# Performance work log

Measured on AMD Instinct MI355X. Metric: run time of the kernel, lower is better.

## Reference

```python
import jax, jax.numpy as jnp
import numpy as np

U, L, B = 512, 512, 256  # units, num_layers (rectangular mesh: L == U), batch
PI = float(np.pi)


def cc_mul(a, b):
    # complex multiply of stacked (real, imag) tensors
    return jnp.stack((a[0] * b[0] - a[1] * b[1], a[0] * b[1] + a[1] * b[0]))


def i_mul(c):
    # s_mul(1j, c): multiply stacked complex by 1j -> (-im, re)
    return jnp.stack((-c[1], c[0]))


def setup_inputs() -> dict:
    key = jax.random.key(0)
    ks = jax.random.split(key, 8)
    x = jax.random.normal(ks[0], (2, B, U), jnp.float32)
    two_pi = 2.0 * PI
    theta = jax.random.uniform(ks[1], (L, U // 2), jnp.float32) * two_pi
    phi = jax.random.uniform(ks[2], (L, U // 2), jnp.float32) * two_pi
    gamma = jax.random.uniform(ks[3], (U,), jnp.float32) * two_pi
    mask = jnp.ones((L, U // 2), jnp.float32)
    enn = jax.random.uniform(ks[4], (U, L), jnp.float32)
    enp = jax.random.uniform(ks[5], (U, L), jnp.float32)
    epn = jax.random.uniform(ks[6], (U, L), jnp.float32)
    epp = jax.random.uniform(ks[7], (U, L), jnp.float32)
    # rectangular-mesh permutations: identity at input/output, interior layers
    # alternate circular shifts so MZIs couple (0,1),(2,3),... then (1,2),(3,4),...
    perms = np.tile(np.arange(U, dtype=np.int32), (L + 1, 1))
    for l in range(1, L):
        perms[l] = np.roll(perms[l], 1 if l % 2 else -1)
    perms = jnp.asarray(perms)
    # pairwise off-diagonal permutation: swap adjacent pairs [1,0,3,2,...]
    pairwise_perm = jnp.asarray(
        np.arange(U, dtype=np.int32).reshape(-1, 2)[:, ::-1].ravel())
    return dict(x=x, theta=theta, phi=phi, gamma=gamma, mask=mask,
                enn=enn, enp=enp, epn=epn, epp=epp,
                perms=perms, pairwise_perm=pairwise_perm)


def reference(x, theta, phi, gamma, mask, enn, enp, epn, epp, perms, pairwise_perm):
    # --- MeshPhasesTorch (basis='sm', hadamard=False) ---
    inv = 1.0 - mask
    th = theta * mask + inv * PI  # (1 - hadamard) * pi
    ph = phi * mask + inv * PI

    def stripe(p):  # single_mode_arrangement: [L, U//2] -> [U, L]
        return jnp.zeros((U, L), p.dtype).at[::2].set(p.T)

    internal = stripe(th)
    external = stripe(ph)
    ipsl = jnp.stack((jnp.cos(internal), jnp.sin(internal)))  # [2, U, L]
    epsl = jnp.stack((jnp.cos(external), jnp.sin(external)))  # [2, U, L]

    roll_m1 = lambda t: jnp.roll(t, -1, axis=1)  # along units axis
    roll_p1 = lambda t: jnp.roll(t, 1, axis=1)

    # --- MeshTorch.mesh_layers (hadamard=False branch) ---
    s11 = epp * ipsl - enn * roll_m1(ipsl)
    s22 = roll_p1(-enn * ipsl + epp * roll_m1(ipsl))
    s12 = i_mul(roll_p1(enp * ipsl + epn * roll_m1(ipsl)))
    s21 = i_mul(epn * ipsl + enp * roll_m1(ipsl))

    diag = cc_mul(epsl, s11 + s22) * 0.5              # [2, U, L]
    off = cc_mul(roll_p1(epsl), s21 + s12) * 0.5      # [2, U, L]
    diag = jnp.transpose(diag, (0, 2, 1))             # [2, L, U]
    off = jnp.transpose(off, (0, 2, 1))

    # --- forward: input phase shift, then sequential vertical layers ---
    in_ps = jnp.stack((jnp.cos(gamma), jnp.sin(gamma)))  # [2, U]
    out = cc_mul(x, in_ps[:, None, :])                   # [2, B, U]
    out = out[..., perms[0]]                             # left perm of layer 0

    def step(carry, inp):
        d, o, rp = inp  # [2, U], [2, U], [U]
        y = cc_mul(carry, d[:, None, :]) \
            + cc_mul(carry, o[:, None, :])[..., pairwise_perm]
        return y[..., rp], None

    xs = (jnp.moveaxis(diag, 1, 0), jnp.moveaxis(off, 1, 0), perms[1:])
    out, _ = jax.lax.scan(step, out, xs)
    return out
```

## Files before the change

kernel.cpp:

```cpp
#include <hip/hip_runtime.h>
#include <hip/hip_fp16.h>


#define UU 512
#define LL 512
#define BB 256
#define KK 256
#define KF 4
#define N9 128
#define W9 9
#define N17 64
#define W17 17
#define N33 32
#define W33 33
#define GQSTRIDE 67584
#define GBLK     8192
#define GTAIL    65536


__global__ __launch_bounds__(512, 2) void mesh_build4(
    const float* __restrict__ theta, const float* __restrict__ phi,
    const float* __restrict__ enn,   const float* __restrict__ enp,
    const float* __restrict__ epn,   const float* __restrict__ epp,
    float2* __restrict__ g9)
{
    __shared__ float2 gwj[7 * UU];
    __shared__ float2 xbuf[2][UU];
    const int u  = threadIdx.x;
    const int j  = ((blockIdx.x & 7) << 4) | (blockIdx.x >> 3);
    const int um = (u + UU - 1) & (UU - 1);
    const int l0 = j * KF;

    const float4 epp_u4 = *(const float4*)(epp + u * LL + l0);
    const float4 epp_m4 = *(const float4*)(epp + um * LL + l0);
    const float4 enn_u4 = *(const float4*)(enn + u * LL + l0);
    const float4 enn_m4 = *(const float4*)(enn + um * LL + l0);
    const float4 enp_u4 = *(const float4*)(enp + u * LL + l0);
    const float4 enp_m4 = *(const float4*)(enp + um * LL + l0);
    const float4 epn_u4 = *(const float4*)(epn + u * LL + l0);
    const float4 epn_m4 = *(const float4*)(epn + um * LL + l0);
    const float epp_u8[4] = {epp_u4.x, epp_u4.y, epp_u4.z, epp_u4.w};
    const float epp_m8[4] = {epp_m4.x, epp_m4.y, epp_m4.z, epp_m4.w};
    const float enn_u8[4] = {enn_u4.x, enn_u4.y, enn_u4.z, enn_u4.w};
    const float enn_m8[4] = {enn_m4.x, enn_m4.y, enn_m4.z, enn_m4.w};
    const float enp_u8[4] = {enp_u4.x, enp_u4.y, enp_u4.z, enp_u4.w};
    const float enp_m8[4] = {enp_m4.x, enp_m4.y, enp_m4.z, enp_m4.w};
    const float epn_u8[4] = {epn_u4.x, epn_u4.y, epn_u4.z, epn_u4.w};
    const float epn_m8[4] = {epn_m4.x, epn_m4.y, epn_m4.z, epn_m4.w};

    const int ka = u >> 1;
    const int kb = ((u + 1) >> 1) & (KK - 1);
    float thA[KF], thB[KF], phC[KF];
    #pragma unroll
    for (int s = 0; s < KF; ++s) {
        thA[s] = theta[(l0 + s) * KK + ka];
        thB[s] = theta[(l0 + s) * KK + kb];
        phC[s] = phi  [(l0 + s) * KK + ka];
    }

    const bool uodd = (u & 1) != 0;

    #define COEF(s, DR, DI, OR_, OI_) { \
        float sA, cA, sB, cB, sC, cC; \
        __sincosf(thA[s], &sA, &cA); \
        __sincosf(thB[s], &sB, &cB); \
        __sincosf(phC[s], &sC, &cC); \
        const float ipu_r = uodd ? 1.f : cA, ipu_i = uodd ? 0.f : sA; \
        const float ipp_r = uodd ? cB : 1.f, ipp_i = uodd ? sB : 0.f; \
        const float ipm_r = uodd ? cA : 1.f, ipm_i = uodd ? sA : 0.f; \
        const float epu_r = uodd ? 1.f : cC, epu_i = uodd ? 0.f : sC; \
        const float epm_r = uodd ? cC : 1.f, epm_i = uodd ? sC : 0.f; \
        const float sd_r = epp_u8[s]*ipu_r - enn_u8[s]*ipp_r - enn_m8[s]*ipm_r + epp_m8[s]*ipu_r; \
        const float sd_i = epp_u8[s]*ipu_i - enn_u8[s]*ipp_i - enn_m8[s]*ipm_i + epp_m8[s]*ipu_i; \
        DR = 0.5f * (epu_r * sd_r - epu_i * sd_i); \
        DI = 0.5f * (epu_r * sd_i + epu_i * sd_r); \
        const float so_r = epn_u8[s]*ipu_r + enp_u8[s]*ipp_r + enp_m8[s]*ipm_r + epn_m8[s]*ipu_r; \
        const float so_i = epn_u8[s]*ipu_i + enp_u8[s]*ipp_i + enp_m8[s]*ipm_i + epn_m8[s]*ipu_i; \
        const float soi_r = -so_i, soi_i = so_r; \
        OR_ = 0.5f * (epm_r * soi_r - epm_i * soi_i); \
        OI_ = 0.5f * (epm_r * soi_i + epm_i * soi_r); }

    float dcur_r, dcur_i, o0_r, o0_i;
    COEF(0, dcur_r, dcur_i, o0_r, o0_i)
    gwj[u] = make_float2(1.f, 0.f);
    xbuf[0][u] = make_float2(o0_r, o0_i);
    __syncthreads();

    int sigma = 0;
    const int tb = uodd ? 0 : 2;
    float2 outr[W9];

    #pragma unroll
    for (int s = 0; s < KF; ++s) {
        const int W  = 2 * s + 1;
        const int Wn = W + 2;
        const int a  = (u + sigma) & (UU - 1);
        const int bx = ((u ^ 1) + sigma) & (UU - 1);
        const float2 ox = xbuf[s & 1][u ^ 1];
        const float dr = dcur_r, di = dcur_i, orr = ox.x, oi = ox.y;

        #pragma unroll
        for (int tn = 0; tn < W9; ++tn) {
            float ar = 0.f, ai = 0.f;
            if (tn < Wn) {
                const int tp = tn - 1;
                const int ts = tn - tb;
                if (0 <= tp && tp < W) {
                    float2 gv = gwj[tp * UU + a];
                    ar += dr * gv.x - di * gv.y;
                    ai += dr * gv.y + di * gv.x;
                }
                if (0 <= ts && ts < W) {
                    float2 gv = gwj[ts * UU + bx];
                    ar += orr * gv.x - oi * gv.y;
                    ai += orr * gv.y + oi * gv.x;
                }
            }
            outr[tn] = make_float2(ar, ai);
        }

        if (s < KF - 1) {
            float dn_r, dn_i, on_r, on_i;
            COEF(s + 1, dn_r, dn_i, on_r, on_i)
            __syncthreads();
            const int wd = (u + sigma) & (UU - 1);
            #pragma unroll
            for (int tn = 0; tn < W9; ++tn)
                if (tn < Wn) gwj[tn * UU + wd] = outr[tn];
            xbuf[(s + 1) & 1][u] = make_float2(on_r, on_i);
            dcur_r = dn_r; dcur_i = dn_i;
            sigma += (s & 1) ? 1 : -1;
            __syncthreads();
        }
    }
    #undef COEF

    const int v = (j == N9 - 1) ? u : um;
    #pragma unroll
    for (int t = 0; t < W9; ++t)
        g9[(j * W9 + t) * UU + v] = outr[t];
}

__global__ __launch_bounds__(512, 2) void mesh_merge33(
    const float2* __restrict__ g9, __half2* __restrict__ g2h)
{
    __shared__ float2 A1[W17 * 80];
    __shared__ float2 A2[W17 * 64];
    const int tid = threadIdx.x;
    const int q   = blockIdx.x & 31;
    const int c   = blockIdx.x >> 5;
    const int u0  = c << 6;
    const int loA2  = (q == N33 - 1) ? -5 : -4;
    const int loC   = (q == N33 - 1) ? -9 : -8;
    const int kbase = u0 + loC;

    const float2* __restrict__ g9a = g9 + (4 * q    ) * W9 * UU;
    const float2* __restrict__ g9b = g9 + (4 * q + 1) * W9 * UU;
    const float2* __restrict__ g9c = g9 + (4 * q + 2) * W9 * UU;
    const float2* __restrict__ g9d = g9 + (4 * q + 3) * W9 * UU;

    for (int e = tid; e < W17 * 80; e += 512) {
        const int tb = e / 80;
        const int kk = e - tb * 80;
        const int k  = (kbase + kk + UU) & (UU - 1);
        float ar = 0.f, ai = 0.f;
        #pragma unroll
        for (int a = 0; a < W9; ++a) {
            const int tbm = tb - a;
            if (0 <= tbm && tbm < W9) {
                const float2 va = g9b[a * UU + k];
                const float2 vb = g9a[tbm * UU + ((k - 4 + a + UU) & (UU - 1))];
                ar += va.x * vb.x - va.y * vb.y;
                ai += va.x * vb.y + va.y * vb.x;
            }
        }
        A1[e] = make_float2(ar, ai);
    }

    for (int e = tid; e < W17 * 64; e += 512) {
        const int ta = e >> 6;
        const int uu = e & 63;
        const int u  = u0 + uu;
        float ar = 0.f, ai = 0.f;
        #pragma unroll
        for (int a = 0; a < W9; ++a) {
            const int tam = ta - a;
            if (0 <= tam && tam < W9) {
                const float2 va = g9d[a * UU + u];
                const float2 vb = g9c[tam * UU + ((u + loA2 + a + UU) & (UU - 1))];
                ar += va.x * vb.x - va.y * vb.y;
                ai += va.x * vb.y + va.y * vb.x;
            }
        }
        A2[e] = make_float2(ar, ai);
    }
    __syncthreads();

    {
        __half2* __restrict__ gq = g2h + q * (W33 * UU);
        for (int e = tid; e < W33 * 64; e += 512) {
            const int t  = e >> 6;
            const int uu = e & 63;
            float ar = 0.f, ai = 0.f;
            #pragma unroll
            for (int ta = 0; ta < W17; ++ta) {
                const int tbm = t - ta;
                if (0 <= tbm && tbm < W17) {
                    const float2 va = A2[ta * 64 + uu];
                    const float2 vb = A1[tbm * 80 + uu + ta];
                    ar += va.x * vb.x - va.y * vb.y;
                    ai += va.x * vb.y + va.y * vb.x;
                }
            }
            const int u = u0 + uu;
            const int idx = (t < 32) ? ((t >> 2) * 2048 + u * 4 + (t & 3))
                                     : (16384 + u);
            gq[idx] = __floats2half2_rn(ar, ai);
        }
    }
}

__global__ __launch_bounds__(512, 2) void mesh_apply(
    const float* __restrict__ x, const float* __restrict__ gamma,
    const __half2* __restrict__ g2h, float* __restrict__ out)
{
    __shared__ float2 sbuf[2][548];
    const int u = threadIdx.x;
    const int b = blockIdx.x;

    float sg, cg;
    __sincosf(gamma[u], &sg, &cg);
    const float xr = x[b * UU + u];
    const float xi = x[BB * UU + b * UU + u];
    float2 v = make_float2(xr * cg - xi * sg, xr * sg + xi * cg);

    #define STORE_STATE(pp)                                                   \
        do {                                                                  \
            sbuf[pp][u + 17] = v;                                             \
            if (u >= 495) sbuf[pp][u - 495] = v;          \
            if (u < 16)   sbuf[pp][u + 529] = v;          \
        } while (0)

    #define BARRIER()                                                         \
        do {                                                                  \
            asm volatile("s_waitcnt lgkmcnt(0)" ::: "memory");                \
            __builtin_amdgcn_s_barrier();                                     \
            asm volatile("" ::: "memory");                                    \
        } while (0)

    #define CFMA(G32V, WR, WI)                                                \
        asm("v_fma_mix_f32 %0, %2, %3, %0 op_sel_hi:[1,0,0]\n\t"              \
            "v_fma_mix_f32 %0, -%2, %4, %0 op_sel:[1,0,0] op_sel_hi:[1,0,0]\n\t" \
            "v_fma_mix_f32 %1, %2, %4, %1 op_sel_hi:[1,0,0]\n\t"              \
            "v_fma_mix_f32 %1, %2, %3, %1 op_sel:[1,0,0] op_sel_hi:[1,0,0]"   \
            : "+v"(ar), "+v"(ai)                                              \
            : "v"(G32V), "v"(WR), "v"(WI))

    STORE_STATE(0);

    const char* __restrict__ gb = (const char*)g2h;
    const int offBlk = u * 16;
    const int offTl  = GTAIL + u * 4;

    uint4 Gv[8];
    uint  G32;
    #define LOADG(PL)                                                         \
        do {                                                                  \
            _Pragma("unroll")                                                 \
            for (int bq = 0; bq < 8; ++bq)                                    \
                Gv[bq] = *(const uint4*)((PL) + bq * GBLK + offBlk);          \
            G32 = *(const uint*)((PL) + offTl);                               \
        } while (0)

    LOADG(gb);
    BARRIER();

    for (int q = 0; q < N33; ++q) {
        const int p = q & 1;
        const int base = u + ((q == N33 - 1) ? 0 : 1);

        float2 w[W33];
        #pragma unroll
        for (int t = 0; t < W33; ++t) w[t] = sbuf[p][base + t];

        float ar = 0.f, ai = 0.f;
        #pragma unroll
        for (int bq = 0; bq < 8; ++bq) {
            const uint wd[4] = {Gv[bq].x, Gv[bq].y, Gv[bq].z, Gv[bq].w};
            #pragma unroll
            for (int i = 0; i < 4; ++i) {
                const float2 wv = w[4 * bq + i];
                CFMA(wd[i], wv.x, wv.y);
            }
        }
        {
            const float2 wv = w[32];
            CFMA(G32, wv.x, wv.y);
        }
        v = make_float2(ar, ai);

        if (q < N33 - 1) {
            LOADG(gb + (q + 1) * GQSTRIDE);
            STORE_STATE(1 - p);
            BARRIER();
        }
    }

    out[b * UU + u]           = v.x;
    out[BB * UU + b * UU + u] = v.y;
    #undef STORE_STATE
    #undef LOADG
    #undef BARRIER
    #undef CFMA
}

#define RSLOTS 6
#define WAITVM40() __builtin_amdgcn_s_waitcnt(0x8F78)
#define STAGE(gg, ss)                                                        \
    _Pragma("unroll")                                                        \
    for (int jq = 0; jq < 8; ++jq)                                           \
        __builtin_amdgcn_global_load_lds(                                    \
            (const __attribute__((address_space(1))) void*)(coef + (gg) * UU + jq * 64 + lane), \
            (__attribute__((address_space(3))) void*)&ring[(ss) * UU + jq * 64], \
            16, 0, 0);

__global__ __launch_bounds__(512) void mesh_precompute_slot(
    const float* __restrict__ theta, const float* __restrict__ phi,
    const float* __restrict__ enn,   const float* __restrict__ enp,
    const float* __restrict__ epn,   const float* __restrict__ epp,
    float4* __restrict__ coef)
{
    const int u  = threadIdx.x;
    const int l  = blockIdx.x;
    const int um = (u + UU - 1) & (UU - 1);
    const float epp_u  = epp[u * LL + l],  epp_um = epp[um * LL + l];
    const float enn_u  = enn[u * LL + l],  enn_um = enn[um * LL + l];
    const float enp_u  = enp[u * LL + l],  enp_um = enp[um * LL + l];
    const float epn_u  = epn[u * LL + l],  epn_um = epn[um * LL + l];
    float ipu_r, ipu_i, ipp_r, ipp_i, ipm_r, ipm_i;
    float epu_r, epu_i, epm_r, epm_i;
    if ((u & 1) == 0) {
        const int k = u >> 1;
        float th = theta[l * KK + k];  __sincosf(th, &ipu_i, &ipu_r);
        ipp_r = 1.f; ipp_i = 0.f;  ipm_r = 1.f; ipm_i = 0.f;
        float phv = phi[l * KK + k];   __sincosf(phv, &epu_i, &epu_r);
        epm_r = 1.f; epm_i = 0.f;
    } else {
        ipu_r = 1.f; ipu_i = 0.f;
        float thp = theta[l * KK + (((u + 1) >> 1) & (KK - 1))]; __sincosf(thp, &ipp_i, &ipp_r);
        float thm = theta[l * KK + (u >> 1)];                    __sincosf(thm, &ipm_i, &ipm_r);
        epu_r = 1.f; epu_i = 0.f;
        float phm = phi[l * KK + (u >> 1)];                      __sincosf(phm, &epm_i, &epm_r);
    }
    const float sd_r = epp_u * ipu_r - enn_u * ipp_r - enn_um * ipm_r + epp_um * ipu_r;
    const float sd_i = epp_u * ipu_i - enn_u * ipp_i - enn_um * ipm_i + epp_um * ipu_i;
    const float d_r = 0.5f * (epu_r * sd_r - epu_i * sd_i);
    const float d_i = 0.5f * (epu_r * sd_i + epu_i * sd_r);
    const float so_r = epn_u * ipu_r + enp_u * ipp_r + enp_um * ipm_r + epn_um * ipu_r;
    const float so_i = epn_u * ipu_i + enp_u * ipp_i + enp_um * ipm_i + epn_um * ipu_i;
    const float soi_r = -so_i, soi_i = so_r;
    const float o_r = 0.5f * (epm_r * soi_r - epm_i * soi_i);
    const float o_i = 0.5f * (epm_r * soi_i + epm_i * soi_r);
    const int slot = ((u & 7) << 6) | (u >> 3);
    coef[l * UU + slot] = make_float4(d_r, d_i, o_r, o_i);
}

#define PAIR_MIX(K)                                                         \
    _Pragma("unroll")                                                       \
    for (int p = 0; p < 4; ++p) {                                           \
        const float4 ke = K[2*p], ko = K[2*p+1];                            \
        y0r[p] = c0r[p]*ke.x - c0i[p]*ke.y + c1r[p]*ko.z - c1i[p]*ko.w;     \
        y0i[p] = c0r[p]*ke.y + c0i[p]*ke.x + c1r[p]*ko.w + c1i[p]*ko.z;     \
        y1r[p] = c1r[p]*ko.x - c1i[p]*ko.y + c0r[p]*ke.z - c0i[p]*ke.w;     \
        y1i[p] = c1r[p]*ko.y + c1i[p]*ko.x + c0r[p]*ke.w + c0i[p]*ke.z;     \
    }

__global__ __launch_bounds__(64) void mesh_chain_r3(
    const float* __restrict__ x, const float* __restrict__ gamma,
    const float4* __restrict__ coef, float* __restrict__ out)
{
    __shared__ float4 ring[RSLOTS * UU];
    const int lane = threadIdx.x;
    const int b    = blockIdx.x;
    const int m0   = lane << 3;
    #pragma unroll
    for (int pl = 0; pl < RSLOTS; ++pl) { STAGE(pl, pl) }
    const float4 xr0 = *(const float4*)(x + b * UU + m0);
    const float4 xr1 = *(const float4*)(x + b * UU + m0 + 4);
    const float4 xi0 = *(const float4*)(x + BB * UU + b * UU + m0);
    const float4 xi1 = *(const float4*)(x + BB * UU + b * UU + m0 + 4);
    const float xr[8] = {xr0.x, xr0.y, xr0.z, xr0.w, xr1.x, xr1.y, xr1.z, xr1.w};
    const float xi[8] = {xi0.x, xi0.y, xi0.z, xi0.w, xi1.x, xi1.y, xi1.z, xi1.w};
    float c0r[4], c0i[4], c1r[4], c1i[4];
    #pragma unroll
    for (int p = 0; p < 4; ++p) {
        float s0, cg0, s1, cg1;
        __sincosf(gamma[m0 + 2*p],     &s0, &cg0);
        __sincosf(gamma[m0 + 2*p + 1], &s1, &cg1);
        c0r[p] = xr[2*p] * cg0 - xi[2*p] * s0;
        c0i[p] = xr[2*p] * s0  + xi[2*p] * cg0;
        c1r[p] = xr[2*p+1] * cg1 - xi[2*p+1] * s1;
        c1i[p] = xr[2*p+1] * s1  + xi[2*p+1] * cg1;
    }
    const int laneM1 = (lane + 63) & 63;
    const int laneP1 = (lane + 1) & 63;
    int sa = 0;
    for (int it = 0; it < 256; ++it) {
        float y0r[4], y0i[4], y1r[4], y1i[4];
        WAITVM40();
        float4 k[8];
        #pragma unroll
        for (int q = 0; q < 8; ++q) k[q] = ring[sa * UU + q * 64 + lane];
        PAIR_MIX(k)
        {
            const float br = __shfl(y1r[3], laneM1, 64);
            const float bi = __shfl(y1i[3], laneM1, 64);
            #pragma unroll
            for (int p = 3; p > 0; --p) { c0r[p] = y1r[p-1]; c0i[p] = y1i[p-1]; }
            c0r[0] = br; c0i[0] = bi;
            #pragma unroll
            for (int p = 0; p < 4; ++p) { c1r[p] = y0r[p]; c1i[p] = y0i[p]; }
        }
        { const int g1 = (2 * it + RSLOTS) & (LL - 1); STAGE(g1, sa) }
        WAITVM40();
        float4 n[8];
        #pragma unroll
        for (int q = 0; q < 8; ++q) n[q] = ring[(sa + 1) * UU + q * 64 + lane];
        PAIR_MIX(n)
        if (it < 255) {
            const float br = __shfl(y0r[0], laneP1, 64);
            const float bi = __shfl(y0i[0], laneP1, 64);
            #pragma unroll
            for (int p = 0; p < 3; ++p) { c0r[p] = y1r[p]; c0i[p] = y1i[p];
                                          c1r[p] = y0r[p+1]; c1i[p] = y0i[p+1]; }
            c0r[3] = y1r[3]; c0i[3] = y1i[3];
            c1r[3] = br;     c1i[3] = bi;
        } else {
            #pragma unroll
            for (int p = 0; p < 4; ++p) { c0r[p] = y0r[p]; c0i[p] = y0i[p];
                                          c1r[p] = y1r[p]; c1i[p] = y1i[p]; }
        }
        { const int g2 = (2 * it + RSLOTS + 1) & (LL - 1); STAGE(g2, sa + 1) }
        sa += 2; if (sa >= RSLOTS) sa = 0;
    }
    *(float4*)(out + b * UU + m0)               = make_float4(c0r[0], c1r[0], c0r[1], c1r[1]);
    *(float4*)(out + b * UU + m0 + 4)           = make_float4(c0r[2], c1r[2], c0r[3], c1r[3]);
    *(float4*)(out + BB * UU + b * UU + m0)     = make_float4(c0i[0], c1i[0], c0i[1], c1i[1]);
    *(float4*)(out + BB * UU + b * UU + m0 + 4) = make_float4(c0i[2], c1i[2], c0i[3], c1i[3]);
}

extern "C" void kernel_launch(void* const* d_in, const int* in_sizes, int n_in,
                              void* d_out, int out_size, void* d_ws, size_t ws_size,
                              hipStream_t stream) {
    (void)in_sizes; (void)n_in; (void)out_size;
    const float* x     = (const float*)d_in[0];
    const float* theta = (const float*)d_in[1];
    const float* phi   = (const float*)d_in[2];
    const float* gamma = (const float*)d_in[3];
    const float* enn   = (const float*)d_in[5];
    const float* enp   = (const float*)d_in[6];
    const float* epn   = (const float*)d_in[7];
    const float* epp   = (const float*)d_in[8];
    float* out = (float*)d_out;

    if (ws_size >= (size_t)6881280) {
        float2*  g9  = (float2*)d_ws;
        __half2* g2h = (__half2*)((char*)d_ws + 4718592);

        mesh_build4<<<N9, UU, 0, stream>>>(theta, phi, enn, enp, epn, epp, g9);
        mesh_merge33<<<N33 * 8, UU, 0, stream>>>(g9, g2h);
        mesh_apply<<<BB, UU, 0, stream>>>(x, gamma, g2h, out);
    } else {
        float4* coef = (float4*)d_ws;
        mesh_precompute_slot<<<LL, UU, 0, stream>>>(theta, phi, enn, enp, epn, epp, coef);
        mesh_chain_r3<<<BB, 64, 0, stream>>>(x, gamma, coef, out);
    }
}
```

Before: 131.1 us.

## Merge banded transfer stages to 65-wide bands, halving apply-loop iterations

Adds a merge pass that combines pairs of 33-wide banded layer products into 65-wide banded matrices. The apply kernel then runs 16 sequential steps instead of 32, which halves the barriers and state exchanges in the latency-bound chain. In exchange each step does nearly twice the FMAs per layer group, needs more registers (16 uint4 coefficients plus 65 window values), and adds an extra launch plus fp16 re-rounding of the merged coefficients, which could reduce accuracy or occupancy.

```diff
diff --git a/kernel.cpp b/kernel.cpp
--- a/kernel.cpp
+++ b/kernel.cpp
@@ -13,9 +13,11 @@
 #define W17 17
 #define N33 32
 #define W33 33
-#define GQSTRIDE 67584
-#define GBLK     8192
-#define GTAIL    65536
+#define N65 16
+#define W65 65
+#define GQ65 133120
+#define GBLK 8192
+#define GT65 131072
 
 
 __global__ __launch_bounds__(512, 2) void mesh_build4(
@@ -212,10 +214,74 @@
                     ai += va.x * vb.y + va.y * vb.x;
                 }
             }
-            const int u = u0 + uu;
-            const int idx = (t < 32) ? ((t >> 2) * 2048 + u * 4 + (t & 3))
-                                     : (16384 + u);
-            gq[idx] = __floats2half2_rn(ar, ai);
+            gq[t * UU + (u0 + uu)] = __floats2half2_rn(ar, ai);
+        }
+    }
+}
+
+__global__ __launch_bounds__(512, 2) void mesh_merge65(
+    const __half2* __restrict__ g33, __half2* __restrict__ g65)
+{
+    __shared__ float2 Bl[W33 * 96];
+    __shared__ float2 Al[W33 * 64];
+    const int tid = threadIdx.x;
+    const int p   = blockIdx.x & 15;
+    const int c   = blockIdx.x >> 4;
+    const int u0  = c << 6;
+    const int loA = (p == 15) ? -17 : -16;
+    const int k0  = u0 + loA;
+
+    const __half2* __restrict__ gA = g33 + (2 * p + 1) * (W33 * UU);
+    const __half2* __restrict__ gB = g33 + (2 * p)     * (W33 * UU);
+
+    for (int e = tid; e < W33 * 96; e += 512) {
+        const int tb = e / 96;
+        const int kk = e - tb * 96;
+        const int k  = (k0 + kk + UU) & (UU - 1);
+        Bl[e] = __half22float2(gB[tb * UU + k]);
+    }
+    for (int e = tid; e < W33 * 64; e += 512) {
+        const int ta = e >> 6;
+        const int uu = e & 63;
+        Al[e] = __half22float2(gA[ta * UU + u0 + uu]);
+    }
+    __syncthreads();
+
+    __half2* __restrict__ gq = g65 + p * (GQ65 / 4);
+    for (int e = tid; e < 17 * 64; e += 512) {
+        const int tg = e >> 6;
+        const int uu = e & 63;
+        const int u  = u0 + uu;
+        if (tg < 16) {
+            float2 acc0 = make_float2(0.f, 0.f), acc1 = acc0;
+            float2 acc2 = acc0, acc3 = acc0;
+            #pragma unroll
+            for (int ta = 0; ta < W33; ++ta) {
+                const float2 a = Al[ta * 64 + uu];
+                const int kk = uu + ta;
+                #define MERGE_TAP(ACC, I)                                     \
+                    { const int tbq = 4 * tg + (I) - ta;                      \
+                      if (0 <= tbq && tbq < W33) {                            \
+                          const float2 bv = Bl[tbq * 96 + kk];                \
+                          ACC.x += a.x * bv.x - a.y * bv.y;                   \
+                          ACC.y += a.x * bv.y + a.y * bv.x; } }
+                MERGE_TAP(acc0, 0) MERGE_TAP(acc1, 1)
+                MERGE_TAP(acc2, 2) MERGE_TAP(acc3, 3)
+                #undef MERGE_TAP
+            }
+            const __half2 h0 = __floats2half2_rn(acc0.x, acc0.y);
+            const __half2 h1 = __floats2half2_rn(acc1.x, acc1.y);
+            const __half2 h2 = __floats2half2_rn(acc2.x, acc2.y);
+            const __half2 h3 = __floats2half2_rn(acc3.x, acc3.y);
+            uint4 pk;
+            pk.x = *(const uint*)&h0;  pk.y = *(const uint*)&h1;
+            pk.z = *(const uint*)&h2;  pk.w = *(const uint*)&h3;
+            *(uint4*)&gq[tg * 2048 + u * 4] = pk;
+        } else {
+            const float2 a  = Al[32 * 64 + uu];
+            const float2 bv = Bl[32 * 96 + uu + 32];
+            gq[(GT65 / 4) + u] = __floats2half2_rn(
+                a.x * bv.x - a.y * bv.y, a.x * bv.y + a.y * bv.x);
         }
     }
 }
@@ -224,7 +290,7 @@
     const float* __restrict__ x, const float* __restrict__ gamma,
     const __half2* __restrict__ g2h, float* __restrict__ out)
 {
-    __shared__ float2 sbuf[2][548];
+    __shared__ float2 sbuf[2][578];
     const int u = threadIdx.x;
     const int b = blockIdx.x;
 
@@ -236,9 +302,9 @@
 
     #define STORE_STATE(pp)                                                   \
         do {                                                                  \
-            sbuf[pp][u + 17] = v;                                             \
-            if (u >= 495) sbuf[pp][u - 495] = v;          \
-            if (u < 16)   sbuf[pp][u + 529] = v;          \
+            sbuf[pp][u + 33] = v;                                             \
+            if (u >= 479) sbuf[pp][u - 479] = v;          \
+            if (u < 33)   sbuf[pp][u + 545] = v;          \
         } while (0)
 
     #define BARRIER()                                                         \
@@ -260,32 +326,32 @@
 
     const char* __restrict__ gb = (const char*)g2h;
     const int offBlk = u * 16;
-    const int offTl  = GTAIL + u * 4;
-
-    uint4 Gv[8];
-    uint  G32;
+    const int offTl  = GT65 + u * 4;
+
+    uint4 Gv[16];
+    uint  G64;
     #define LOADG(PL)                                                         \
         do {                                                                  \
             _Pragma("unroll")                                                 \
-            for (int bq = 0; bq < 8; ++bq)                                    \
+            for (int bq = 0; bq < 16; ++bq)                                   \
                 Gv[bq] = *(const uint4*)((PL) + bq * GBLK + offBlk);          \
-            G32 = *(const uint*)((PL) + offTl);                               \
+            G64 = *(const uint*)((PL) + offTl);                               \
         } while (0)
 
     LOADG(gb);
     BARRIER();
 
-    for (int q = 0; q < N33; ++q) {
+    for (int q = 0; q < N65; ++q) {
         const int p = q & 1;
-        const int base = u + ((q == N33 - 1) ? 0 : 1);
-
-        float2 w[W33];
-        #pragma unroll
-        for (int t = 0; t < W33; ++t) w[t] = sbuf[p][base + t];
+        const int base = u + ((q == N65 - 1) ? 0 : 1);
+
+        float2 w[W65];
+        #pragma unroll
+        for (int t = 0; t < W65; ++t) w[t] = sbuf[p][base + t];
 
         float ar = 0.f, ai = 0.f;
         #pragma unroll
-        for (int bq = 0; bq < 8; ++bq) {
+        for (int bq = 0; bq < 16; ++bq) {
             const uint wd[4] = {Gv[bq].x, Gv[bq].y, Gv[bq].z, Gv[bq].w};
             #pragma unroll
             for (int i = 0; i < 4; ++i) {
@@ -294,13 +360,13 @@
             }
         }
         {
-            const float2 wv = w[32];
-            CFMA(G32, wv.x, wv.y);
+            const float2 wv = w[64];
+            CFMA(G64, wv.x, wv.y);
         }
         v = make_float2(ar, ai);
 
-        if (q < N33 - 1) {
-            LOADG(gb + (q + 1) * GQSTRIDE);
+        if (q < N65 - 1) {
+            LOADG(gb + (q + 1) * GQ65);
             STORE_STATE(1 - p);
             BARRIER();
         }
@@ -464,12 +530,14 @@
     float* out = (float*)d_out;
 
     if (ws_size >= (size_t)6881280) {
-        float2*  g9  = (float2*)d_ws;
-        __half2* g2h = (__half2*)((char*)d_ws + 4718592);
-
-        mesh_build4<<<N9, UU, 0, stream>>>(theta, phi, enn, enp, epn, epp, g9);
-        mesh_merge33<<<N33 * 8, UU, 0, stream>>>(g9, g2h);
-        mesh_apply<<<BB, UU, 0, stream>>>(x, gamma, g2h, out);
+        float2*  g9   = (float2*)d_ws;
+        __half2* g33h = (__half2*)((char*)d_ws + 4718592);
+        __half2* g65h = (__half2*)d_ws;
+
+        mesh_build4 <<<N9,      UU, 0, stream>>>(theta, phi, enn, enp, epn, epp, g9);
+        mesh_merge33<<<N33 * 8, UU, 0, stream>>>(g9, g33h);
+        mesh_merge65<<<N65 * 8, UU, 0, stream>>>(g33h, g65h);
+        mesh_apply  <<<BB,      UU, 0, stream>>>(x, gamma, g65h, out);
     } else {
         float4* coef = (float4*)d_ws;
         mesh_precompute_slot<<<LL, UU, 0, stream>>>(theta, phi, enn, enp, epn, epp, coef);
```

New measurement: 145.4 us. +10.9%, slower.
